# Kernel tuning notes

Measured on AMD Instinct MI355X. Metric: run time of the kernel, lower is better.

Reference implementation:

```python
import jax, jax.numpy as jnp
import numpy as np

N_NODES = 100000
N_EDGES = 800000
D_IN = 128
D_H = 512


def _glorot(key, shape):
    fan_in, fan_out = shape[1], shape[0]
    lim = jnp.sqrt(6.0 / (fan_in + fan_out))
    return jax.random.uniform(key, shape, jnp.float32, -lim, lim)


def setup_inputs() -> dict:
    key = jax.random.key(0)
    ks = jax.random.split(key, 16)
    x = jax.random.normal(ks[0], (N_NODES, D_IN), jnp.float32)
    edge_index = jax.random.randint(ks[1], (2, N_EDGES), 0, N_NODES, jnp.int64)
    return {
        "x": x,
        "edge_index": edge_index,
        # SAGEConv layer1: lin_l (neighbors, with bias), lin_r (root, no bias)
        "Wl1": _glorot(ks[2], (D_H, D_IN)), "bl1": jnp.zeros((D_H,), jnp.float32),
        "Wr1": _glorot(ks[3], (D_H, D_IN)),
        # SAGEConv layer2
        "Wl2": _glorot(ks[4], (D_H, D_H)), "bl2": jnp.zeros((D_H,), jnp.float32),
        "Wr2": _glorot(ks[5], (D_H, D_H)),
        # SAGEConv layer3
        "Wl3": _glorot(ks[6], (D_H, D_H)), "bl3": jnp.zeros((D_H,), jnp.float32),
        "Wr3": _glorot(ks[7], (D_H, D_H)),
        # residual projections W, W2 (nn.Linear with bias)
        "Ww": _glorot(ks[8], (D_H, D_IN)), "bw": jnp.zeros((D_H,), jnp.float32),
        "Ww2": _glorot(ks[9], (D_H, D_IN)), "bw2": jnp.zeros((D_H,), jnp.float32),
        # shared PReLU parameter (nn.PReLU default: single param init 0.25)
        "a": jnp.array(0.25, jnp.float32),
    }


def _prelu(x, a):
    return jnp.where(x > 0, x, a * x)


def _sage_conv(x, src, dst, Wl, bl, Wr):
    # mean-aggregate neighbor features x[src] onto dst, then linear + root term
    msg = jax.ops.segment_sum(x[src], dst, num_segments=N_NODES)  # [N, d]
    deg = jax.ops.segment_sum(jnp.ones((src.shape[0],), x.dtype), dst,
                              num_segments=N_NODES)
    agg = msg / jnp.maximum(deg, 1.0)[:, None]
    return agg @ Wl.T + bl + x @ Wr.T


def reference(x, edge_index, Wl1, bl1, Wr1, Wl2, bl2, Wr2, Wl3, bl3, Wr3,
              Ww, bw, Ww2, bw2, a):
    src, dst = edge_index[0], edge_index[1]
    h1 = _prelu(_sage_conv(x, src, dst, Wl1, bl1, Wr1), a)
    h2 = _prelu(_sage_conv(h1 + (x @ Ww.T + bw), src, dst, Wl2, bl2, Wr2), a)
    h3 = _prelu(_sage_conv(h2 + h1 + (x @ Ww2.T + bw2), src, dst, Wl3, bl3, Wr3), a)
    return h3
```

## Files before the change

kernel.cpp:

```cpp
#include <hip/hip_runtime.h>
#include <stddef.h>

#define NN 100000
#define NE 800000
#define DIN 128
#define DH 512
#define MT 782
#define NWG (MT * 4)
#define CPX (NWG / 8)

typedef __attribute__((ext_vector_type(8))) short sh8;
typedef __attribute__((ext_vector_type(4))) float f32x4;

__device__ __forceinline__ unsigned short f2b(float f) {
  unsigned u = __float_as_uint(f);
  return (unsigned short)((u + 0x7FFFu + ((u >> 16) & 1u)) >> 16);
}
__device__ __forceinline__ float b2f(unsigned short s) {
  return __uint_as_float(((unsigned)s) << 16);
}

__device__ __forceinline__ void gload16(const unsigned short* g, unsigned short* l) {
  __builtin_amdgcn_global_load_lds(
      (const __attribute__((address_space(1))) void*)g,
      (__attribute__((address_space(3))) void*)l, 16, 0, 0);
}

#define SCHED_FENCE() __builtin_amdgcn_sched_barrier(0)
#define MEM_FENCE() asm volatile("" ::: "memory")
#define VMCNT(n) asm volatile("s_waitcnt vmcnt(" #n ")" ::: "memory")



__global__ void k_count(const int* __restrict__ dst, int* __restrict__ cnt) {
  int i = blockIdx.x * blockDim.x + threadIdx.x;
  if (i < NE) atomicAdd(&cnt[dst[i]], 1);
}

__global__ void k_invdeg(const int* __restrict__ cnt, float* __restrict__ inv_deg) {
  int i = blockIdx.x * blockDim.x + threadIdx.x;
  if (i < NN) inv_deg[i] = 1.0f / (float)(cnt[i] > 1 ? cnt[i] : 1);
}

__global__ void k_scan1(const int* __restrict__ cnt, int* __restrict__ excl,
                        int* __restrict__ partials) {
  __shared__ int sh[256];
  int tid = threadIdx.x;
  int base = blockIdx.x * 1024 + tid * 4;
  int v[4]; int s = 0;
#pragma unroll
  for (int i = 0; i < 4; i++) { int idx = base + i; v[i] = (idx < NN) ? cnt[idx] : 0; s += v[i]; }
  sh[tid] = s; __syncthreads();
  for (int off = 1; off < 256; off <<= 1) {
    int t = (tid >= off) ? sh[tid - off] : 0;
    __syncthreads();
    sh[tid] += t;
    __syncthreads();
  }
  int run = sh[tid] - s;
#pragma unroll
  for (int i = 0; i < 4; i++) { int idx = base + i; if (idx < NN) excl[idx] = run; run += v[i]; }
  if (tid == 255) partials[blockIdx.x] = sh[255];
}

__global__ void k_scan2(int* __restrict__ partials, int* __restrict__ row_start, int nparts) {
  __shared__ int sh[128];
  int tid = threadIdx.x;
  int v = (tid < nparts) ? partials[tid] : 0;
  sh[tid] = v; __syncthreads();
  for (int off = 1; off < 128; off <<= 1) {
    int t = (tid >= off) ? sh[tid - off] : 0;
    __syncthreads();
    sh[tid] += t;
    __syncthreads();
  }
  if (tid < nparts) partials[tid] = sh[tid] - v;
  if (tid == 127) row_start[NN] = sh[127];
}

__global__ void k_scan3(int* __restrict__ excl, const int* __restrict__ partials) {
  int i = blockIdx.x * blockDim.x + threadIdx.x;
  if (i < NN) excl[i] += partials[i >> 10];
}

__global__ void k_fill(const int* __restrict__ src, const int* __restrict__ dst,
                       const int* __restrict__ row_start, int* __restrict__ cursor,
                       int* __restrict__ ssrc) {
  int i = blockIdx.x * blockDim.x + threadIdx.x;
  if (i < NE) {
    int d = dst[i];
    int pos = atomicAdd(&cursor[d], 1);
    ssrc[row_start[d] + pos] = src[i];
  }
}


__global__ void k_f2b(const float* __restrict__ src, unsigned short* __restrict__ dst, int n) {
  int i = (blockIdx.x * blockDim.x + threadIdx.x) * 4;
  if (i < n) {
    float4 v = *(const float4*)(src + i);
    ushort4 o;
    o.x = f2b(v.x); o.y = f2b(v.y); o.z = f2b(v.z); o.w = f2b(v.w);
    *(ushort4*)(dst + i) = o;
  }
}


__global__ __launch_bounds__(256) void k_aggb512(
    const unsigned short* __restrict__ z, const int* __restrict__ rs,
    const int* __restrict__ ssrc, const float* __restrict__ inv_deg,
    unsigned short* __restrict__ agg) {
  int w = (blockIdx.x * blockDim.x + threadIdx.x) >> 6;
  int lane = threadIdx.x & 63;
  if (w >= NN) return;
  int e0 = rs[w], e1 = rs[w + 1];
  float acc[8] = {0, 0, 0, 0, 0, 0, 0, 0};
  int e = e0;
  for (; e + 3 < e1; e += 4) {
    int s0i = ssrc[e], s1i = ssrc[e + 1], s2i = ssrc[e + 2], s3i = ssrc[e + 3];
    sh8 v0 = *(const sh8*)(z + (size_t)s0i * DH + lane * 8);
    sh8 v1 = *(const sh8*)(z + (size_t)s1i * DH + lane * 8);
    sh8 v2 = *(const sh8*)(z + (size_t)s2i * DH + lane * 8);
    sh8 v3 = *(const sh8*)(z + (size_t)s3i * DH + lane * 8);
#pragma unroll
    for (int j = 0; j < 8; ++j)
      acc[j] += (b2f((unsigned short)v0[j]) + b2f((unsigned short)v1[j])) +
                (b2f((unsigned short)v2[j]) + b2f((unsigned short)v3[j]));
  }
  for (; e < e1; ++e) {
    int sa = ssrc[e];
    sh8 va = *(const sh8*)(z + (size_t)sa * DH + lane * 8);
#pragma unroll
    for (int j = 0; j < 8; ++j) acc[j] += b2f((unsigned short)va[j]);
  }
  float s0 = inv_deg[w];
  sh8 o;
#pragma unroll
  for (int j = 0; j < 8; ++j) o[j] = (short)f2b(acc[j] * s0);
  *(sh8*)(agg + (size_t)w * DH + lane * 8) = o;
}

__global__ __launch_bounds__(256) void k_aggb128(
    const unsigned short* __restrict__ z, const int* __restrict__ rs,
    const int* __restrict__ ssrc, const float* __restrict__ inv_deg,
    unsigned short* __restrict__ agg) {
  int w = (blockIdx.x * blockDim.x + threadIdx.x) >> 6;
  int lane = threadIdx.x & 63;
  if (w >= NN) return;
  int e0 = rs[w], e1 = rs[w + 1];
  float a0 = 0.f, a1 = 0.f;
  int e = e0;
  for (; e + 3 < e1; e += 4) {
    unsigned v0 = *(const unsigned*)(z + (size_t)ssrc[e] * DIN + lane * 2);
    unsigned v1 = *(const unsigned*)(z + (size_t)ssrc[e + 1] * DIN + lane * 2);
    unsigned v2 = *(const unsigned*)(z + (size_t)ssrc[e + 2] * DIN + lane * 2);
    unsigned v3 = *(const unsigned*)(z + (size_t)ssrc[e + 3] * DIN + lane * 2);
    a0 += (b2f((unsigned short)(v0 & 0xFFFFu)) + b2f((unsigned short)(v1 & 0xFFFFu))) +
          (b2f((unsigned short)(v2 & 0xFFFFu)) + b2f((unsigned short)(v3 & 0xFFFFu)));
    a1 += (b2f((unsigned short)(v0 >> 16)) + b2f((unsigned short)(v1 >> 16))) +
          (b2f((unsigned short)(v2 >> 16)) + b2f((unsigned short)(v3 >> 16)));
  }
  for (; e < e1; ++e) {
    unsigned va = *(const unsigned*)(z + (size_t)ssrc[e] * DIN + lane * 2);
    a0 += b2f((unsigned short)(va & 0xFFFFu));
    a1 += b2f((unsigned short)(va >> 16));
  }
  float s0 = inv_deg[w];
  unsigned o = (unsigned)f2b(a0 * s0) | ((unsigned)f2b(a1 * s0) << 16);
  *(unsigned*)(agg + (size_t)w * DIN + lane * 2) = o;
}


__device__ __forceinline__ void stage_tile(
    unsigned short* ldsA, unsigned short* ldsB,
    const unsigned short* __restrict__ A, int sA, int m0,
    const unsigned short* __restrict__ B, int sB, int n0,
    int k0, int tid) {
  const int w = tid >> 6, l = tid & 63;
  const int kc = (((l & 3) ^ ((l >> 3) & 3)) * 8);
  const int rsub = l >> 2;
#pragma unroll
  for (int i = 0; i < 2; ++i) {
    int rl = w * 32 + i * 16 + rsub;
    int ra = m0 + rl; if (ra >= NN) ra = NN - 1;
    gload16(A + (size_t)ra * sA + k0 + kc, ldsA + (size_t)(w * 32 + i * 16) * 32);
    gload16(B + (size_t)(n0 + rl) * sB + k0 + kc, ldsB + (size_t)(w * 32 + i * 16) * 32);
  }
}

__device__ __forceinline__ void mfma_step(
    const unsigned short* As, const unsigned short* Bs,
    int wr, int wc, int r16, int sw, f32x4 (&acc)[4][4]) {
  sh8 af[4], bf[4];
#pragma unroll
  for (int i = 0; i < 4; ++i)
    af[i] = *(const sh8*)&As[(wr + i * 16 + r16) * 32 + sw * 8];
#pragma unroll
  for (int j = 0; j < 4; ++j)
    bf[j] = *(const sh8*)&Bs[(wc + j * 16 + r16) * 32 + sw * 8];
#pragma unroll
  for (int i = 0; i < 4; ++i)
#pragma unroll
    for (int j = 0; j < 4; ++j)
      acc[i][j] = __builtin_amdgcn_mfma_f32_16x16x32_bf16(af[i], bf[j], acc[i][j], 0, 0, 0);
}

#define PIPE_WAIT(s, S)                 \
  do {                                  \
    if ((s) < (S) - 2) VMCNT(8);        \
    else if ((s) == (S) - 2) VMCNT(4);  \
    else VMCNT(0);                      \
    SCHED_FENCE();                      \
    __builtin_amdgcn_s_barrier();       \
    MEM_FENCE(); SCHED_FENCE();         \
  } while (0)

#define PIPE_END()                      \
  do {                                  \
    SCHED_FENCE();                      \
    __builtin_amdgcn_s_barrier();       \
    MEM_FENCE(); SCHED_FENCE();         \
  } while (0)

__global__ __launch_bounds__(256, 2) void k_gemm1(
    const unsigned short* __restrict__ ag, const unsigned short* __restrict__ xb,
    const unsigned short* __restrict__ Wl1, const unsigned short* __restrict__ Wr1,
    const unsigned short* __restrict__ Ww, const unsigned short* __restrict__ Ww2,
    const float* __restrict__ bl1, const float* __restrict__ bw,
    const float* __restrict__ bw2, const float* __restrict__ aptr,
    unsigned short* __restrict__ z2o, unsigned short* __restrict__ z3po) {
  __shared__ __align__(16) unsigned short As[3][128 * 32];
  __shared__ __align__(16) unsigned short Bs[3][128 * 32];
  const int tid = threadIdx.x;
  const int b = blockIdx.x;
  const int L = (b & 7) * CPX + (b >> 3);
  const int m0 = (L >> 2) * 128, n0 = (L & 3) * 128;
  const int wid = tid >> 6, lane = tid & 63;
  const int r16 = lane & 15, kg = lane >> 4;
  const int swz = kg ^ ((r16 >> 1) & 3);
  const int wr = (wid >> 1) * 64, wc = (wid & 1) * 64;

  f32x4 a0[4][4], a1[4][4], a2[4][4];
#pragma unroll
  for (int i = 0; i < 4; ++i)
#pragma unroll
    for (int j = 0; j < 4; ++j) { a0[i][j] = 0.f; a1[i][j] = 0.f; a2[i][j] = 0.f; }

  auto stage = [&](int s, int buf) {
    const int seg = s >> 2, k0 = (s & 3) * 32;
    const unsigned short* Ap = (seg == 0) ? ag : xb;
    const unsigned short* Bp = (seg == 0) ? Wl1 : (seg == 1) ? Wr1 : (seg == 2) ? Ww : Ww2;
    stage_tile(As[buf], Bs[buf], Ap, DIN, m0, Bp, DIN, n0, k0, tid);
  };

  stage(0, 0);
  stage(1, 1);
  int cur = 0, nxt = 2;
  for (int s = 0; s < 16; ++s) {
    if (s + 2 < 16) stage(s + 2, nxt);
    PIPE_WAIT(s, 16);
    const int seg = s >> 2;
    __builtin_amdgcn_s_setprio(1);
    if (seg <= 1)      mfma_step(As[cur], Bs[cur], wr, wc, r16, swz, a0);
    else if (seg == 2) mfma_step(As[cur], Bs[cur], wr, wc, r16, swz, a1);
    else               mfma_step(As[cur], Bs[cur], wr, wc, r16, swz, a2);
    __builtin_amdgcn_s_setprio(0);
    PIPE_END();
    cur = (cur == 2) ? 0 : cur + 1;
    nxt = (nxt == 2) ? 0 : nxt + 1;
  }

  const float aval = aptr[0];
#pragma unroll
  for (int i = 0; i < 4; ++i) {
    const int mbase = m0 + wr + i * 16 + kg * 4;
#pragma unroll
    for (int j = 0; j < 4; ++j) {
      const int col = n0 + wc + j * 16 + r16;
      const float b1 = bl1[col], b2 = bw[col], b3 = bw2[col];
#pragma unroll
      for (int r = 0; r < 4; ++r) {
        const int m = mbase + r;
        if (m >= NN) continue;
        float h1 = a0[i][j][r] + b1;
        h1 = h1 > 0.f ? h1 : aval * h1;
        z2o[(size_t)m * DH + col] = f2b(h1 + a1[i][j][r] + b2);
        z3po[(size_t)m * DH + col] = f2b(h1 + a2[i][j][r] + b3);
      }
    }
  }
}


template <bool LAST>
__global__ __launch_bounds__(256) void k_rg23(
    const unsigned short* __restrict__ Aag, const unsigned short* __restrict__ Az,
    const unsigned short* __restrict__ Wl, const unsigned short* __restrict__ Wr,
    const float* __restrict__ bl, const float* __restrict__ aptr,
    const unsigned short* __restrict__ z3p, void* __restrict__ outp) {
  __shared__ __align__(16) unsigned short As[2][128 * 32];
  __shared__ __align__(16) unsigned short Bs[2][128 * 32];
  const int tid = threadIdx.x;
  const int b = blockIdx.x;
  const int L = (b & 7) * CPX + (b >> 3);
  const int m0 = (L >> 2) * 128, n0 = (L & 3) * 128;
  const int wid = tid >> 6, lane = tid & 63;
  const int r16 = lane & 15, kg = lane >> 4;
  const int swz = kg ^ ((r16 >> 1) & 3);
  const int wr = (wid >> 1) * 64, wc = (wid & 1) * 64;
  const int rA = tid >> 2;
  const int cA = (tid & 3) * 8;
  const int cW = (((tid & 3) ^ ((tid >> 3) & 3)) * 8);

  f32x4 acc[4][4];
#pragma unroll
  for (int i = 0; i < 4; ++i)
#pragma unroll
    for (int j = 0; j < 4; ++j) acc[i][j] = 0.f;

  const int rowA0 = (m0 + rA < NN) ? m0 + rA : NN - 1;
  const int rowA1 = (m0 + rA + 64 < NN) ? m0 + rA + 64 : NN - 1;
  const size_t oA0 = (size_t)rowA0 * DH + cA;
  const size_t oA1 = (size_t)rowA1 * DH + cA;
  const size_t oB0 = (size_t)(n0 + rA) * DH + cA;
  const size_t oB1 = (size_t)(n0 + rA + 64) * DH + cA;

  sh8 va0 = *(const sh8*)(Aag + oA0);
  sh8 va1 = *(const sh8*)(Aag + oA1);
  sh8 vb0 = *(const sh8*)(Wl + oB0);
  sh8 vb1 = *(const sh8*)(Wl + oB1);

#pragma unroll
  for (int s = 0; s < 32; ++s) {
    unsigned short* Aw = As[s & 1];
    unsigned short* Bw = Bs[s & 1];
    *(sh8*)&Aw[rA * 32 + cW] = va0;
    *(sh8*)&Aw[(rA + 64) * 32 + cW] = va1;
    *(sh8*)&Bw[rA * 32 + cW] = vb0;
    *(sh8*)&Bw[(rA + 64) * 32 + cW] = vb1;
    __syncthreads();
    if (s + 1 < 32) {
      const int t = s + 1;
      const unsigned short* A = (t < 16) ? Aag : Az;
      const unsigned short* W = (t < 16) ? Wl : Wr;
      const int ko = (t & 15) * 32;
      va0 = *(const sh8*)(A + oA0 + ko);
      va1 = *(const sh8*)(A + oA1 + ko);
      vb0 = *(const sh8*)(W + oB0 + ko);
      vb1 = *(const sh8*)(W + oB1 + ko);
    }
    mfma_step(Aw, Bw, wr, wc, r16, swz, acc);
  }

  const float aval = aptr[0];
  float* outf = (float*)outp;
  unsigned short* outb = (unsigned short*)outp;
#pragma unroll
  for (int i = 0; i < 4; ++i) {
    const int mbase = m0 + wr + i * 16 + kg * 4;
#pragma unroll
    for (int j = 0; j < 4; ++j) {
      const int col = n0 + wc + j * 16 + r16;
      const float bv = bl[col];
#pragma unroll
      for (int r = 0; r < 4; ++r) {
        const int m = mbase + r;
        if (m >= NN) continue;
        float h = acc[i][j][r] + bv;
        h = h > 0.f ? h : aval * h;
        if constexpr (LAST) {
          outf[(size_t)m * DH + col] = h;
        } else {
          outb[(size_t)m * DH + col] = f2b(h + b2f(z3p[(size_t)m * DH + col]));
        }
      }
    }
  }
}


extern "C" void kernel_launch(void* const* d_in, const int* in_sizes, int n_in,
                              void* d_out, int out_size, void* d_ws, size_t ws_size,
                              hipStream_t stream) {
  const float* x = (const float*)d_in[0];
  const int* ei = (const int*)d_in[1];
  const float* Wl1 = (const float*)d_in[2];
  const float* bl1 = (const float*)d_in[3];
  const float* Wr1 = (const float*)d_in[4];
  const float* Wl2 = (const float*)d_in[5];
  const float* bl2 = (const float*)d_in[6];
  const float* Wr2 = (const float*)d_in[7];
  const float* Wl3 = (const float*)d_in[8];
  const float* bl3 = (const float*)d_in[9];
  const float* Wr3 = (const float*)d_in[10];
  const float* Ww  = (const float*)d_in[11];
  const float* bw  = (const float*)d_in[12];
  const float* Ww2 = (const float*)d_in[13];
  const float* bw2 = (const float*)d_in[14];
  const float* ap  = (const float*)d_in[15];
  float* out = (float*)d_out;

  const size_t MP = 100096;
  char* w = (char*)d_ws;
  size_t off = 0;
  unsigned short* xb   = (unsigned short*)(w + off); off += MP * DIN * 2;
  unsigned short* ag1  = (unsigned short*)(w + off); off += MP * DIN * 2;
  unsigned short* agb  = (unsigned short*)(w + off); off += MP * DH * 2;
  unsigned short* zb   = (unsigned short*)(w + off); off += MP * DH * 2;
  unsigned short* zc   = (unsigned short*)(w + off); off += MP * DH * 2;
  unsigned short* z3pb = (unsigned short*)(w + off); off += MP * DH * 2;
  unsigned short* Wl1b = (unsigned short*)(w + off); off += (size_t)DH * DIN * 2;
  unsigned short* Wr1b = (unsigned short*)(w + off); off += (size_t)DH * DIN * 2;
  unsigned short* Wwb  = (unsigned short*)(w + off); off += (size_t)DH * DIN * 2;
  unsigned short* Ww2b = (unsigned short*)(w + off); off += (size_t)DH * DIN * 2;
  unsigned short* Wl2b = (unsigned short*)(w + off); off += (size_t)DH * DH * 2;
  unsigned short* Wr2b = (unsigned short*)(w + off); off += (size_t)DH * DH * 2;
  unsigned short* Wl3b = (unsigned short*)(w + off); off += (size_t)DH * DH * 2;
  unsigned short* Wr3b = (unsigned short*)(w + off); off += (size_t)DH * DH * 2;
  float* inv_deg = (float*)(w + off); off += (size_t)NN * 4;
  int* row_start = (int*)(w + off); off += (size_t)(NN + 1) * 4;
  int* cursor = (int*)(w + off); off += (size_t)NN * 4;
  int* ssrc = (int*)(w + off); off += (size_t)NE * 4;
  int* partials = (int*)(w + off); off += 512;

  const int* esrc = ei;
  const int* edst = ei + NE;

  hipMemsetAsync(cursor, 0, NN * 4, stream);
  k_count<<<(NE + 255) / 256, 256, 0, stream>>>(edst, cursor);
  k_invdeg<<<(NN + 255) / 256, 256, 0, stream>>>(cursor, inv_deg);
  k_scan1<<<(NN + 1023) / 1024, 256, 0, stream>>>(cursor, row_start, partials);
  k_scan2<<<1, 128, 0, stream>>>(partials, row_start, (NN + 1023) / 1024);
  k_scan3<<<(NN + 255) / 256, 256, 0, stream>>>(row_start, partials);
  hipMemsetAsync(cursor, 0, NN * 4, stream);
  k_fill<<<(NE + 255) / 256, 256, 0, stream>>>(esrc, edst, row_start, cursor, ssrc);

  const int WK = DH * DIN;
  const int WB = DH * DH;
  k_f2b<<<(WK / 4 + 255) / 256, 256, 0, stream>>>(Wl1, Wl1b, WK);
  k_f2b<<<(WK / 4 + 255) / 256, 256, 0, stream>>>(Wr1, Wr1b, WK);
  k_f2b<<<(WK / 4 + 255) / 256, 256, 0, stream>>>(Ww,  Wwb,  WK);
  k_f2b<<<(WK / 4 + 255) / 256, 256, 0, stream>>>(Ww2, Ww2b, WK);
  k_f2b<<<(WB / 4 + 255) / 256, 256, 0, stream>>>(Wl2, Wl2b, WB);
  k_f2b<<<(WB / 4 + 255) / 256, 256, 0, stream>>>(Wr2, Wr2b, WB);
  k_f2b<<<(WB / 4 + 255) / 256, 256, 0, stream>>>(Wl3, Wl3b, WB);
  k_f2b<<<(WB / 4 + 255) / 256, 256, 0, stream>>>(Wr3, Wr3b, WB);
  k_f2b<<<(NN * DIN / 4 + 255) / 256, 256, 0, stream>>>(x, xb, NN * DIN);

  k_aggb128<<<(NN + 3) / 4, 256, 0, stream>>>(xb, row_start, ssrc, inv_deg, ag1);
  k_gemm1<<<NWG, 256, 0, stream>>>(ag1, xb, Wl1b, Wr1b, Wwb, Ww2b, bl1, bw, bw2, ap,
                                   zb, z3pb);
  k_aggb512<<<(NN + 3) / 4, 256, 0, stream>>>(zb, row_start, ssrc, inv_deg, agb);
  k_rg23<false><<<NWG, 256, 0, stream>>>(agb, zb, Wl2b, Wr2b, bl2, ap, z3pb, zc);
  k_aggb512<<<(NN + 3) / 4, 256, 0, stream>>>(zc, row_start, ssrc, inv_deg, agb);
  k_rg23<true><<<NWG, 256, 0, stream>>>(agb, zc, Wl3b, Wr3b, bl3, ap, nullptr, out);
}
```

Baseline: 982.8 us.

## Replace layer-2 GEMM with per-wave 64x64 register-tiled kernel without LDS

Adds k_wv23, in which each wavefront independently computes a 64x64 output tile. It loads A and W fragments straight from global memory into registers, double-buffered across 32 K-steps, and issues 16 MFMAs per step. The LDS staging and workgroup-level sharing of the old k_rg23 are gone, which removes LDS traffic and barriers. The cost is that operand reuse across waves is lost and the kernel depends on L2/L1 for reuse. Only layer 2 uses the new kernel; layer 3 keeps the old one.

```diff
diff --git a/kernel.cpp b/kernel.cpp
--- a/kernel.cpp
+++ b/kernel.cpp
@@ -29,7 +29,6 @@
 #define SCHED_FENCE() __builtin_amdgcn_sched_barrier(0)
 #define MEM_FENCE() asm volatile("" ::: "memory")
 #define VMCNT(n) asm volatile("s_waitcnt vmcnt(" #n ")" ::: "memory")
-
 
 
 __global__ void k_count(const int* __restrict__ dst, int* __restrict__ cnt) {
@@ -361,6 +360,102 @@
 #pragma unroll
     for (int j = 0; j < 4; ++j) {
       const int col = n0 + wc + j * 16 + r16;
+      const float bv = bl[col];
+#pragma unroll
+      for (int r = 0; r < 4; ++r) {
+        const int m = mbase + r;
+        if (m >= NN) continue;
+        float h = acc[i][j][r] + bv;
+        h = h > 0.f ? h : aval * h;
+        if constexpr (LAST) {
+          outf[(size_t)m * DH + col] = h;
+        } else {
+          outb[(size_t)m * DH + col] = f2b(h + b2f(z3p[(size_t)m * DH + col]));
+        }
+      }
+    }
+  }
+}
+
+
+__device__ __forceinline__ void mfma16(const sh8 (&af)[4], const sh8 (&bf)[4],
+                                       f32x4 (&acc)[4][4]) {
+#pragma unroll
+  for (int i = 0; i < 4; ++i)
+#pragma unroll
+    for (int j = 0; j < 4; ++j)
+      acc[i][j] = __builtin_amdgcn_mfma_f32_16x16x32_bf16(af[i], bf[j], acc[i][j], 0, 0, 0);
+}
+
+template <bool LAST>
+__global__ __launch_bounds__(256) void k_wv23(
+    const unsigned short* __restrict__ Aag, const unsigned short* __restrict__ Az,
+    const unsigned short* __restrict__ Wl, const unsigned short* __restrict__ Wr,
+    const float* __restrict__ bl, const float* __restrict__ aptr,
+    const unsigned short* __restrict__ z3p, void* __restrict__ outp) {
+  const int tid = threadIdx.x, wid = tid >> 6, lane = tid & 63;
+  const int b = blockIdx.x;
+  const int L = (b & 7) * CPX + (b >> 3);
+  const int task = L * 4 + wid;
+  const int n0 = (task & 7) * 64;
+  const int m0 = (task >> 3) * 64;
+  const int r16 = lane & 15, kg = lane >> 4;
+
+  size_t oA[4], oB[4];
+#pragma unroll
+  for (int i = 0; i < 4; ++i) {
+    int r = m0 + i * 16 + r16; if (r >= NN) r = NN - 1;
+    oA[i] = (size_t)r * DH + kg * 8;
+    oB[i] = (size_t)(n0 + i * 16 + r16) * DH + kg * 8;
+  }
+
+  f32x4 acc[4][4];
+#pragma unroll
+  for (int i = 0; i < 4; ++i)
+#pragma unroll
+    for (int j = 0; j < 4; ++j) acc[i][j] = 0.f;
+
+  sh8 af0[4], bf0[4], af1[4], bf1[4];
+#pragma unroll
+  for (int i = 0; i < 4; ++i) {
+    af0[i] = *(const sh8*)(Aag + oA[i]);
+    bf0[i] = *(const sh8*)(Wl + oB[i]);
+  }
+
+#pragma unroll
+  for (int s = 0; s < 32; ++s) {
+    if (s + 1 < 32) {
+      const int t = s + 1;
+      const unsigned short* A = (t < 16) ? Aag : Az;
+      const unsigned short* W = (t < 16) ? Wl : Wr;
+      const int ko = (t & 15) * 32;
+      if ((s & 1) == 0) {
+#pragma unroll
+        for (int i = 0; i < 4; ++i) {
+          af1[i] = *(const sh8*)(A + oA[i] + ko);
+          bf1[i] = *(const sh8*)(W + oB[i] + ko);
+        }
+      } else {
+#pragma unroll
+        for (int i = 0; i < 4; ++i) {
+          af0[i] = *(const sh8*)(A + oA[i] + ko);
+          bf0[i] = *(const sh8*)(W + oB[i] + ko);
+        }
+      }
+    }
+    if ((s & 1) == 0) mfma16(af0, bf0, acc);
+    else              mfma16(af1, bf1, acc);
+  }
+
+  const float aval = aptr[0];
+  float* outf = (float*)outp;
+  unsigned short* outb = (unsigned short*)outp;
+#pragma unroll
+  for (int i = 0; i < 4; ++i) {
+    const int mbase = m0 + i * 16 + kg * 4;
+#pragma unroll
+    for (int j = 0; j < 4; ++j) {
+      const int col = n0 + j * 16 + r16;
       const float bv = bl[col];
 #pragma unroll
       for (int r = 0; r < 4; ++r) {
@@ -451,7 +546,7 @@
   k_gemm1<<<NWG, 256, 0, stream>>>(ag1, xb, Wl1b, Wr1b, Wwb, Ww2b, bl1, bw, bw2, ap,
                                    zb, z3pb);
   k_aggb512<<<(NN + 3) / 4, 256, 0, stream>>>(zb, row_start, ssrc, inv_deg, agb);
-  k_rg23<false><<<NWG, 256, 0, stream>>>(agb, zb, Wl2b, Wr2b, bl2, ap, z3pb, zc);
+  k_wv23<false><<<NWG, 256, 0, stream>>>(agb, zb, Wl2b, Wr2b, bl2, ap, z3pb, zc);
   k_aggb512<<<(NN + 3) / 4, 256, 0, stream>>>(zc, row_start, ssrc, inv_deg, agb);
   k_rg23<true><<<NWG, 256, 0, stream>>>(agb, zc, Wl3b, Wr3b, bl3, ap, nullptr, out);
 }
```

Result: slower. 1.247 ms (+26.9%).
